# Optimization experiments

Measured on AMD Instinct MI355X. Metric: run time of the kernel, lower is better.

## Reference

```python
import jax, jax.numpy as jnp
import numpy as np
import math

BS, S, D = 2, 2048, 2048
DOWN, UP, H, RD = 512, 1024, 16, 32
HD = D // H            # 128, used only in softmax scale
VD = UP // H           # 64 per-head value dim
CD = UP // H           # 64 per-head content q/k dim
SCALE = math.sqrt(HD) + math.sqrt(RD)


def _rope(x, head_dim):
    # x: [bs, heads, seq, head_dim]; standard rotate-half RoPE
    seq = x.shape[2]
    inv_freq = 1.0 / (10000.0 ** (jnp.arange(0, head_dim, 2, dtype=jnp.float32) / head_dim))
    freqs = jnp.arange(seq, dtype=jnp.float32)[:, None] * inv_freq[None, :]  # [S, hd/2]
    emb = jnp.concatenate([freqs, freqs], axis=-1)                            # [S, hd]
    cos = jnp.cos(emb)[None, None]
    sin = jnp.sin(emb)[None, None]
    x1, x2 = x[..., : head_dim // 2], x[..., head_dim // 2 :]
    rot = jnp.concatenate([-x2, x1], axis=-1)
    return x * cos + rot * sin


def setup_inputs() -> dict:
    key = jax.random.key(0)
    ks = jax.random.split(key, 10)
    sd = 0.02
    inp = {
        'h': jax.random.normal(ks[0], (BS, S, D), jnp.float32),
        'mask': jnp.tril(jnp.ones((1, 1, S, S), jnp.int32)),
        'Wdkv': jax.random.normal(ks[1], (DOWN, D), jnp.float32) * sd,
        'bdkv': jnp.zeros((DOWN,), jnp.float32),
        'Wuk': jax.random.normal(ks[2], (UP, DOWN), jnp.float32) * sd,
        'buk': jnp.zeros((UP,), jnp.float32),
        'Wuv': jax.random.normal(ks[3], (UP, DOWN), jnp.float32) * sd,
        'buv': jnp.zeros((UP,), jnp.float32),
        'Wdq': jax.random.normal(ks[4], (DOWN, D), jnp.float32) * sd,
        'bdq': jnp.zeros((DOWN,), jnp.float32),
        'Wuq': jax.random.normal(ks[5], (UP, DOWN), jnp.float32) * sd,
        'buq': jnp.zeros((UP,), jnp.float32),
        'Wqr': jax.random.normal(ks[6], (RD * H, DOWN), jnp.float32) * sd,
        'bqr': jnp.zeros((RD * H,), jnp.float32),
        'Wkr': jax.random.normal(ks[7], (RD, D), jnp.float32) * sd,
        'bkr': jnp.zeros((RD,), jnp.float32),
        'Wfc': jax.random.normal(ks[8], (D, H * VD), jnp.float32) * sd,
        'bfc': jnp.zeros((D,), jnp.float32),
    }
    return inp


def reference(h, mask, Wdkv, bdkv, Wuk, buk, Wuv, buv, Wdq, bdq, Wuq, buq,
              Wqr, bqr, Wkr, bkr, Wfc, bfc):
    bs, seq, _ = h.shape
    # low-rank KV path
    c_kv = h @ Wdkv.T + bdkv                                   # [bs,S,DOWN]
    k_c = (c_kv @ Wuk.T + buk).reshape(bs, seq, H, CD).transpose(0, 2, 1, 3)
    v_c = (c_kv @ Wuv.T + buv).reshape(bs, seq, H, VD).transpose(0, 2, 1, 3)
    # low-rank Q path
    c_q = h @ Wdq.T + bdq                                      # [bs,S,DOWN]
    q_c = (c_q @ Wuq.T + buq).reshape(bs, seq, H, CD).transpose(0, 2, 1, 3)
    # decoupled RoPE paths
    q_r = _rope((c_q @ Wqr.T + bqr).reshape(bs, seq, H, RD).transpose(0, 2, 1, 3), RD)
    k_r = _rope((h @ Wkr.T + bkr).reshape(bs, seq, 1, RD).transpose(0, 2, 1, 3), RD)
    k_r = jnp.broadcast_to(k_r, (bs, H, seq, RD))              # shared RoPE key across heads
    q = jnp.concatenate([q_c, q_r], axis=-1)                   # [bs,H,S,CD+RD]
    k = jnp.concatenate([k_c, k_r], axis=-1)
    scores = jnp.einsum('bhqd,bhkd->bhqk', q, k)
    # NB: original applies mask BEFORE dividing by scale
    scores = jnp.where(mask == 0, -1e9, scores)
    probs = jax.nn.softmax(scores / SCALE, axis=-1)
    out = jnp.einsum('bhqk,bhkd->bhqd', probs, v_c)            # [bs,H,S,VD]
    out = out.transpose(0, 2, 1, 3).reshape(bs, seq, H * VD)
    return out @ Wfc.T + bfc
```

## Files before the change

### kernel.cpp

```cpp
#include <hip/hip_runtime.h>
#include <hip/hip_bf16.h>
#include <math.h>

typedef unsigned short u16;
typedef __attribute__((ext_vector_type(8))) short bf16x8;
typedef __attribute__((ext_vector_type(4))) float f32x4;
typedef __attribute__((ext_vector_type(16))) float f32x16;

namespace {

constexpr int BS = 2;
constexpr int S = 2048;
constexpr int D = 2048;
constexpr int DOWN = 512;
constexpr int UP = 1024;
constexpr int H = 16;
constexpr int RD = 32;
constexpr int VD = 64;
constexpr int QKD = 96;
constexpr int M = BS * S;
constexpr int N1 = 1152;
constexpr int N2 = 2048;
constexpr int N3 = 1536;

__device__ __forceinline__ float b2f(u16 u) {
  unsigned int x = ((unsigned int)u) << 16;
  return __uint_as_float(x);
}
__device__ __forceinline__ u16 f2b(float f) {
  unsigned int u = __float_as_uint(f);
  u += 0x7fff + ((u >> 16) & 1);
  return (u16)(u >> 16);
}
__device__ __forceinline__ void store_out(float* p, float v) { *p = v; }
__device__ __forceinline__ void store_out(u16* p, float v) { *p = f2b(v); }

__device__ __forceinline__ void async16(const u16* g, u16* lds) {
  __builtin_amdgcn_global_load_lds(
      (const __attribute__((address_space(1))) unsigned int*)g,
      (__attribute__((address_space(3))) unsigned int*)lds, 16, 0, 0);
}

__device__ __forceinline__ float exp2_fast(float x) {
#if __has_builtin(__builtin_amdgcn_exp2f)
  return __builtin_amdgcn_exp2f(x);
#else
  float r;
  asm("v_exp_f32 %0, %1" : "=v"(r) : "v"(x));
  return r;
#endif
}

__device__ __forceinline__ bf16x8 pack8(const float* f) {
  union { __hip_bfloat162 h2[4]; bf16x8 v; } u;
#pragma unroll
  for (int i = 0; i < 4; ++i)
    u.h2[i] = __float22bfloat162_rn(make_float2(f[2 * i], f[2 * i + 1]));
  return u.v;
}

__device__ __forceinline__ f32x4 mfma32(bf16x8 a, bf16x8 b, f32x4 c) {
  return __builtin_amdgcn_mfma_f32_16x16x32_bf16(a, b, c, 0, 0, 0);
}
__device__ __forceinline__ f32x16 mfma3216(bf16x8 a, bf16x8 b, f32x16 c) {
  return __builtin_amdgcn_mfma_f32_32x32x16_bf16(a, b, c, 0, 0, 0);
}

__global__ __launch_bounds__(256) void prep_kernel(
    const float* __restrict__ h, const float* __restrict__ Wdkv,
    const float* __restrict__ Wdq, const float* __restrict__ Wkr,
    const float* __restrict__ Wuk, const float* __restrict__ Wuv,
    const float* __restrict__ Wuq, const float* __restrict__ Wqr,
    const float* __restrict__ Wfc, const float* __restrict__ bdkv,
    const float* __restrict__ bdq, const float* __restrict__ bkr,
    const float* __restrict__ buk, const float* __restrict__ buv,
    const float* __restrict__ buq, const float* __restrict__ bqr,
    u16* __restrict__ hb, u16* __restrict__ Wcat1, u16* __restrict__ Wcat2,
    u16* __restrict__ Wcat3, u16* __restrict__ Wfcb,
    float* __restrict__ bcat1, float* __restrict__ bcat2,
    float* __restrict__ bcat3, float* __restrict__ ct, float* __restrict__ st) {
  const long i = (long)blockIdx.x * 256 + threadIdx.x;
  if (i >= 3630240) return;
  if (i < 3620864) {
    const float* src; u16* dst; long off;
    if      (i < 2097152) { src = h;    dst = hb;              off = i; }
    else if (i < 2359296) { src = Wdkv; dst = Wcat1;           off = i - 2097152; }
    else if (i < 2621440) { src = Wdq;  dst = Wcat1 + 1048576; off = i - 2359296; }
    else if (i < 2637824) { src = Wkr;  dst = Wcat1 + 2097152; off = i - 2621440; }
    else if (i < 2768896) { src = Wuk;  dst = Wcat2;           off = i - 2637824; }
    else if (i < 2899968) { src = Wuv;  dst = Wcat2 + 524288;  off = i - 2768896; }
    else if (i < 3031040) { src = Wuq;  dst = Wcat3;           off = i - 2899968; }
    else if (i < 3096576) { src = Wqr;  dst = Wcat3 + 524288;  off = i - 3031040; }
    else                  { src = Wfc;  dst = Wfcb;            off = i - 3096576; }
    float4 v = ((const float4*)src)[off];
    ushort4 o;
    o.x = f2b(v.x); o.y = f2b(v.y); o.z = f2b(v.z); o.w = f2b(v.w);
    ((ushort4*)dst)[off] = o;
  } else if (i < 3622048) {
    long j0 = (i - 3620864) * 4;
#pragma unroll
    for (int e = 0; e < 4; ++e) {
      long j = j0 + e;
      if (j < N1) {
        float v = 0.f;
        if (j < 512) v = bdkv[j];
        else if (j < 1024) v = bdq[j - 512];
        else if (j < 1056) v = bkr[j - 1024];
        bcat1[j] = v;
      } else if (j < N1 + N2) {
        long jj = j - N1;
        bcat2[jj] = (jj < 1024) ? buk[jj] : buv[jj - 1024];
      } else {
        long jj = j - N1 - N2;
        bcat3[jj] = (jj < 1024) ? buq[jj] : bqr[jj - 1024];
      }
    }
  } else {
    long k0 = (i - 3622048) * 4;
#pragma unroll
    for (int e = 0; e < 4; ++e) {
      long k = k0 + e;
      int s = (int)(k >> 4), r = (int)(k & 15);
      float f = powf(10000.f, -(float)r / 16.f);
      float th = (float)s * f;
      ct[k] = cosf(th);
      st[k] = sinf(th);
    }
  }
}

template <int BN, typename OutT>
__device__ __forceinline__ void gemm_body(
    const u16* __restrict__ A, int lda, const u16* __restrict__ W, int ldw,
    const float* __restrict__ bias, OutT* __restrict__ C, int ldc, int K,
    int m0, int n0) {
  constexpr int NFR = BN / 32;
  __shared__ u16 As[128 * 32];
  __shared__ u16 Bs[BN * 32];
  const int t = threadIdx.x;
  const int lane = t & 63, wave = t >> 6;
  const int wm = (wave >> 1) * 64, wn = (wave & 1) * (BN / 2);
  const int lrow = lane & 15, lk = (lane >> 4) * 8;
  const int srow = lane >> 2, scol = (lane & 3) * 8;
  f32x4 acc[4][NFR] = {};
  for (int k0 = 0; k0 < K; k0 += 32) {
    __syncthreads();
    {
      int r = wave * 32 + srow;
      async16(A + (size_t)(m0 + r) * lda + k0 + scol, As + (wave * 32) * 32);
      async16(A + (size_t)(m0 + r + 16) * lda + k0 + scol,
              As + (wave * 32 + 16) * 32);
    }
    if (BN == 128) {
      int r = wave * 32 + srow;
      async16(W + (size_t)(n0 + r) * ldw + k0 + scol, Bs + (wave * 32) * 32);
      async16(W + (size_t)(n0 + r + 16) * ldw + k0 + scol,
              Bs + (wave * 32 + 16) * 32);
    } else {
      int r = wave * 16 + srow;
      async16(W + (size_t)(n0 + r) * ldw + k0 + scol, Bs + (wave * 16) * 32);
    }
    __syncthreads();
    bf16x8 af[4], bfr[NFR];
#pragma unroll
    for (int i = 0; i < 4; ++i)
      af[i] = *(const bf16x8*)(As + (wm + i * 16 + lrow) * 32 + lk);
#pragma unroll
    for (int i = 0; i < NFR; ++i)
      bfr[i] = *(const bf16x8*)(Bs + (wn + i * 16 + lrow) * 32 + lk);
#pragma unroll
    for (int mi = 0; mi < 4; ++mi)
#pragma unroll
      for (int ni = 0; ni < NFR; ++ni)
        acc[mi][ni] = mfma32(af[mi], bfr[ni], acc[mi][ni]);
  }
#pragma unroll
  for (int mi = 0; mi < 4; ++mi)
#pragma unroll
    for (int ni = 0; ni < NFR; ++ni)
#pragma unroll
      for (int r = 0; r < 4; ++r) {
        int m = m0 + wm + mi * 16 + (lane >> 4) * 4 + r;
        int n = n0 + wn + ni * 16 + lrow;
        store_out(C + (size_t)m * ldc + n, acc[mi][ni][r] + bias[n]);
      }
}

template <int BN, typename OutT>
__global__ __launch_bounds__(256) void gemm_bt_mfma(
    const u16* __restrict__ A, int lda, const u16* __restrict__ W, int ldw,
    const float* __restrict__ bias, OutT* __restrict__ C, int ldc, int K) {
  gemm_body<BN, OutT>(A, lda, W, ldw, bias, C, ldc, K,
                      blockIdx.x * 128, blockIdx.y * BN);
}

__global__ __launch_bounds__(256) void gemm_up_fused(
    const u16* __restrict__ C1v, const u16* __restrict__ Wcat2,
    const u16* __restrict__ Wcat3, const float* __restrict__ bcat2,
    const float* __restrict__ bcat3, u16* __restrict__ C2,
    u16* __restrict__ C3) {
  const int by = blockIdx.y;
  const u16* A;
  const u16* W;
  const float* bias;
  u16* C;
  int ldc, n0;
  if (by < 16) {
    A = C1v; W = Wcat2; bias = bcat2; C = C2; ldc = N2; n0 = by * 128;
  } else {
    A = C1v + DOWN; W = Wcat3; bias = bcat3; C = C3; ldc = N3;
    n0 = (by - 16) * 128;
  }
  gemm_body<128, u16>(A, N1, W, DOWN, bias, C, ldc, DOWN,
                      blockIdx.x * 128, n0);
}

__global__ __launch_bounds__(256) void transpose_kernel(
    const u16* __restrict__ in, int ld_in, u16* __restrict__ outT, int ld_out) {
  __shared__ u16 tile[64][72];
  const int m0 = blockIdx.x * 64, n0 = blockIdx.y * 64;
  const int r = threadIdx.x >> 2, c0 = (threadIdx.x & 3) * 16;
  *(bf16x8*)(&tile[r][c0]) =
      *(const bf16x8*)(in + (size_t)(m0 + r) * ld_in + n0 + c0);
  *(bf16x8*)(&tile[r][c0 + 8]) =
      *(const bf16x8*)(in + (size_t)(m0 + r) * ld_in + n0 + c0 + 8);
  __syncthreads();
  bf16x8 o0, o1;
#pragma unroll
  for (int j = 0; j < 8; ++j) {
    o0[j] = (short)tile[c0 + j][r];
    o1[j] = (short)tile[c0 + 8 + j][r];
  }
  *(bf16x8*)(outT + (size_t)(n0 + r) * ld_out + m0 + c0) = o0;
  *(bf16x8*)(outT + (size_t)(n0 + r) * ld_out + m0 + c0 + 8) = o1;
}

__global__ __launch_bounds__(192) void pack_q_kernel(
    const u16* __restrict__ qc, const u16* __restrict__ qr,
    const float* __restrict__ ct, const float* __restrict__ st,
    u16* __restrict__ Qp) {
  const int t = threadIdx.x;
  const int sub = (t >= 96) ? 1 : 0;
  const int d = t - sub * 96;
  const int s = blockIdx.x * 2 + sub, h = blockIdx.y, b = blockIdx.z;
  const float sc = 1.44269504088896f / (sqrtf(128.f) + sqrtf(32.f));
  float val;
  if (d < 64) {
    val = b2f(qc[(size_t)(b * S + s) * N3 + h * VD + d]);
  } else {
    int r = d - 64;
    const u16* qrow = qr + (size_t)(b * S + s) * N3 + h * RD;
    float x = b2f(qrow[r]), xp = b2f(qrow[r ^ 16]);
    float c = ct[s * 16 + (r & 15)], sn = st[s * 16 + (r & 15)];
    val = (r < 16) ? (x * c - xp * sn) : (x * c + xp * sn);
  }
  Qp[((size_t)(b * H + h) * S + s) * QKD + d] = f2b(val * sc);
}

__global__ __launch_bounds__(192) void pack_k_kernel(
    const u16* __restrict__ kc,
    const u16* __restrict__ kr,
    const float* __restrict__ ct, const float* __restrict__ st,
    u16* __restrict__ Kp) {
  const int t = threadIdx.x;
  const int sub = (t >= 96) ? 1 : 0;
  const int d = t - sub * 96;
  const int s = blockIdx.x * 2 + sub, h = blockIdx.y, b = blockIdx.z;
  float val;
  if (d < 64) {
    val = b2f(kc[(size_t)(b * S + s) * N2 + h * VD + d]);
  } else {
    int r = d - 64;
    const u16* krow = kr + (size_t)(b * S + s) * N1;
    float x = b2f(krow[r]), xp = b2f(krow[r ^ 16]);
    float c = ct[s * 16 + (r & 15)], sn = st[s * 16 + (r & 15)];
    val = (r < 16) ? (x * c - xp * sn) : (x * c + xp * sn);
  }
  Kp[((size_t)(b * H + h) * S + s) * QKD + d] = f2b(val);
}

__global__ __launch_bounds__(256) void attn_mfma(
    const u16* __restrict__ Qp, const u16* __restrict__ Kp,
    const u16* __restrict__ Vt, u16* __restrict__ attnb) {
  const int t = threadIdx.x, wave = t >> 6, lane = t & 63;
  const int l31 = lane & 31, hw = lane >> 5;
  const int bh = blockIdx.x & 31;
  const int b = bh >> 4, h = bh & 15;
  const int j = blockIdx.x >> 5;
  const int qgroup = (j < 8) ? (15 - j) : (j - 8);
  const int q0w = qgroup * 128 + wave * 32;
  const size_t hbo = (size_t)bh * S;

  bf16x8 qf[6];
  {
    const u16* qrow = Qp + (hbo + q0w + l31) * QKD + hw * 8;
#pragma unroll
    for (int c = 0; c < 6; ++c) qf[c] = *(const bf16x8*)(qrow + c * 16);
  }
  f32x16 O0 = {0,0,0,0,0,0,0,0,0,0,0,0,0,0,0,0};
  f32x16 O1 = {0,0,0,0,0,0,0,0,0,0,0,0,0,0,0,0};
  float lsum = 0.f;
  const int q_abs = q0w + l31;
  const u16* vb0 = Vt + ((size_t)(h * VD + l31)) * M + (size_t)b * S + 8 * hw;

  for (int k0 = 0; k0 < q0w + 32; k0 += 32) {
    const u16* kb = Kp + (hbo + k0 + l31) * QKD + hw * 8;
    f32x16 s = {0,0,0,0,0,0,0,0,0,0,0,0,0,0,0,0};
#pragma unroll
    for (int c = 0; c < 6; ++c) {
      bf16x8 kf = *(const bf16x8*)(kb + c * 16);
      s = mfma3216(kf, qf[c], s);
    }
    float e[16];
    if (k0 + 31 > q0w) {
#pragma unroll
      for (int r = 0; r < 16; ++r) {
        int key_abs = k0 + (r & 3) + 8 * (r >> 2) + 4 * hw;
        float v = exp2_fast(s[r]);
        e[r] = (key_abs <= q_abs) ? v : 0.f;
      }
    } else {
#pragma unroll
      for (int r = 0; r < 16; ++r) e[r] = exp2_fast(s[r]);
    }
#pragma unroll
    for (int r = 0; r < 16; ++r) lsum += e[r];
    float x[16];
#pragma unroll
    for (int r = 0; r < 16; ++r) x[r] = __shfl_xor(e[r], 32);
    float f0[8], f1[8];
#pragma unroll
    for (int jj = 0; jj < 4; ++jj) {
      f0[jj]     = hw ? x[jj + 4]  : e[jj];
      f0[jj + 4] = hw ? e[jj + 4]  : x[jj];
      f1[jj]     = hw ? x[jj + 12] : e[jj + 8];
      f1[jj + 4] = hw ? e[jj + 12] : x[jj + 8];
    }
    bf16x8 pa0 = pack8(f0);
    bf16x8 pa1 = pack8(f1);
    bf16x8 vf00 = *(const bf16x8*)(vb0 + k0);
    bf16x8 vf01 = *(const bf16x8*)(vb0 + k0 + 16);
    bf16x8 vf10 = *(const bf16x8*)(vb0 + (size_t)32 * M + k0);
    bf16x8 vf11 = *(const bf16x8*)(vb0 + (size_t)32 * M + k0 + 16);
    O0 = mfma3216(pa0, vf00, O0);
    O0 = mfma3216(pa1, vf01, O0);
    O1 = mfma3216(pa0, vf10, O1);
    O1 = mfma3216(pa1, vf11, O1);
  }

  float tot = lsum + __shfl_xor(lsum, 32);
  u16* ob = attnb + (size_t)b * S * UP + h * VD;
#pragma unroll
  for (int r = 0; r < 16; ++r) {
    int rowq = (r & 3) + 8 * (r >> 2) + 4 * hw;
    float linv = 1.f / __shfl(tot, rowq);
    size_t rowoff = (size_t)(q0w + rowq) * UP;
    ob[rowoff + l31] = f2b(O0[r] * linv);
    ob[rowoff + 32 + l31] = f2b(O1[r] * linv);
  }
}

}

extern "C" void kernel_launch(void* const* d_in, const int* in_sizes, int n_in,
                              void* d_out, int out_size, void* d_ws, size_t ws_size,
                              hipStream_t stream) {
  const float* h    = (const float*)d_in[0];
  const float* Wdkv = (const float*)d_in[2];
  const float* bdkv = (const float*)d_in[3];
  const float* Wuk  = (const float*)d_in[4];
  const float* buk  = (const float*)d_in[5];
  const float* Wuv  = (const float*)d_in[6];
  const float* buv  = (const float*)d_in[7];
  const float* Wdq  = (const float*)d_in[8];
  const float* bdq  = (const float*)d_in[9];
  const float* Wuq  = (const float*)d_in[10];
  const float* buq  = (const float*)d_in[11];
  const float* Wqr  = (const float*)d_in[12];
  const float* bqr  = (const float*)d_in[13];
  const float* Wkr  = (const float*)d_in[14];
  const float* bkr  = (const float*)d_in[15];
  const float* Wfc  = (const float*)d_in[16];
  const float* bfc  = (const float*)d_in[17];
  float* out = (float*)d_out;

  u16* p = (u16*)d_ws;
  u16* hb    = p; p += (size_t)M * D;
  u16* Wcat1 = p; p += (size_t)N1 * D;
  u16* Wcat2 = p; p += (size_t)N2 * DOWN;
  u16* Wcat3 = p; p += (size_t)N3 * DOWN;
  u16* Wfcb  = p; p += (size_t)D * UP;
  u16* C1    = p; p += (size_t)M * N1;
  u16* C2    = p; p += (size_t)M * N2;
  u16* C3    = p; p += (size_t)M * N3;
  u16* Qp    = p; p += 6291456;
  u16* Kp    = p; p += 6291456;
  u16* Vt    = p; p += (size_t)UP * M;
  float* bcat1 = (float*)p; p += 2 * N1;
  float* bcat2 = (float*)p; p += 2 * N2;
  float* bcat3 = (float*)p; p += 2 * N3;
  float* ct = (float*)p; p += 2 * S * 16;
  float* st = (float*)p; p += 2 * S * 16;
  u16* attnb = C1;

  prep_kernel<<<dim3(14181), 256, 0, stream>>>(
      h, Wdkv, Wdq, Wkr, Wuk, Wuv, Wuq, Wqr, Wfc,
      bdkv, bdq, bkr, buk, buv, buq, bqr,
      hb, Wcat1, Wcat2, Wcat3, Wfcb, bcat1, bcat2, bcat3, ct, st);

  gemm_bt_mfma<64, u16><<<dim3(M / 128, N1 / 64), 256, 0, stream>>>(
      hb, D, Wcat1, D, bcat1, C1, N1, D);
  gemm_up_fused<<<dim3(M / 128, 28), 256, 0, stream>>>(
      C1, Wcat2, Wcat3, bcat2, bcat3, C2, C3);

  pack_q_kernel<<<dim3(S / 2, H, BS), 192, 0, stream>>>(
      C3, C3 + UP, ct, st, Qp);
  pack_k_kernel<<<dim3(S / 2, H, BS), 192, 0, stream>>>(
      C2, C1 + 2 * DOWN, ct, st, Kp);
  transpose_kernel<<<dim3(M / 64, UP / 64), 256, 0, stream>>>(
      C2 + UP, N2, Vt, M);

  attn_mfma<<<dim3(512), 256, 0, stream>>>(Qp, Kp, Vt, attnb);

  gemm_bt_mfma<64, float><<<dim3(M / 128, D / 64), 256, 0, stream>>>(
      attnb, UP, Wfcb, UP, bfc, out, D, UP);
}
```

Measured before the change: 363.4 us.

## Split attention keys across waves with LDS reduction and permlane swap

Each block now handles a single 32-query tile, and its four waves take interleaved 32-key chunks. The partial outputs and row sums are combined through shared memory at the end, and the launch grows from 512 to 2048 blocks to raise parallelism and balance the causal workload. The cross-half shuffle used to repack probabilities for the PV MFMA is replaced by bf16 packing plus v_permlane32_swap. K fragments are prefetched one iteration ahead. The cost is an LDS reduction and a block-wide barrier, and each block now reloads the same Q tile, so Q is read redundantly.

```diff
diff --git a/kernel.cpp b/kernel.cpp
--- a/kernel.cpp
+++ b/kernel.cpp
@@ -51,12 +51,13 @@
 #endif
 }
 
-__device__ __forceinline__ bf16x8 pack8(const float* f) {
-  union { __hip_bfloat162 h2[4]; bf16x8 v; } u;
-#pragma unroll
-  for (int i = 0; i < 4; ++i)
-    u.h2[i] = __float22bfloat162_rn(make_float2(f[2 * i], f[2 * i + 1]));
-  return u.v;
+__device__ __forceinline__ unsigned pkbf(float a, float b) {
+  union { __hip_bfloat162 h; unsigned u; } c;
+  c.h = __float22bfloat162_rn(make_float2(a, b));
+  return c.u;
+}
+__device__ __forceinline__ void plswap(unsigned& a, unsigned& b) {
+  asm("v_permlane32_swap_b32 %0, %1" : "+v"(a), "+v"(b));
 }
 
 __device__ __forceinline__ f32x4 mfma32(bf16x8 a, bf16x8 b, f32x4 c) {
@@ -279,17 +280,18 @@
   Kp[((size_t)(b * H + h) * S + s) * QKD + d] = f2b(val);
 }
 
-__global__ __launch_bounds__(256) void attn_mfma(
+__global__ __launch_bounds__(256, 4) void attn_mfma(
     const u16* __restrict__ Qp, const u16* __restrict__ Kp,
     const u16* __restrict__ Vt, u16* __restrict__ attnb) {
   const int t = threadIdx.x, wave = t >> 6, lane = t & 63;
   const int l31 = lane & 31, hw = lane >> 5;
   const int bh = blockIdx.x & 31;
   const int b = bh >> 4, h = bh & 15;
-  const int j = blockIdx.x >> 5;
-  const int qgroup = (j < 8) ? (15 - j) : (j - 8);
-  const int q0w = qgroup * 128 + wave * 32;
+  const int tile = 63 - (blockIdx.x >> 5);
+  const int q0w = tile * 32;
   const size_t hbo = (size_t)bh * S;
+
+  __shared__ float red[3][64][33];
 
   bf16x8 qf[6];
   {
@@ -303,60 +305,83 @@
   const int q_abs = q0w + l31;
   const u16* vb0 = Vt + ((size_t)(h * VD + l31)) * M + (size_t)b * S + 8 * hw;
 
-  for (int k0 = 0; k0 < q0w + 32; k0 += 32) {
-    const u16* kb = Kp + (hbo + k0 + l31) * QKD + hw * 8;
+  bf16x8 kf[6];
+  {
+    const u16* kb = Kp + (hbo + wave * 32 + l31) * QKD + hw * 8;
+#pragma unroll
+    for (int c = 0; c < 6; ++c) kf[c] = *(const bf16x8*)(kb + c * 16);
+  }
+
+  for (int m = wave; m <= tile; m += 4) {
+    const int k0 = m * 32;
     f32x16 s = {0,0,0,0,0,0,0,0,0,0,0,0,0,0,0,0};
 #pragma unroll
-    for (int c = 0; c < 6; ++c) {
-      bf16x8 kf = *(const bf16x8*)(kb + c * 16);
-      s = mfma3216(kf, qf[c], s);
-    }
-    float e[16];
-    if (k0 + 31 > q0w) {
-#pragma unroll
-      for (int r = 0; r < 16; ++r) {
-        int key_abs = k0 + (r & 3) + 8 * (r >> 2) + 4 * hw;
-        float v = exp2_fast(s[r]);
-        e[r] = (key_abs <= q_abs) ? v : 0.f;
-      }
-    } else {
-#pragma unroll
-      for (int r = 0; r < 16; ++r) e[r] = exp2_fast(s[r]);
-    }
-#pragma unroll
-    for (int r = 0; r < 16; ++r) lsum += e[r];
-    float x[16];
-#pragma unroll
-    for (int r = 0; r < 16; ++r) x[r] = __shfl_xor(e[r], 32);
-    float f0[8], f1[8];
-#pragma unroll
-    for (int jj = 0; jj < 4; ++jj) {
-      f0[jj]     = hw ? x[jj + 4]  : e[jj];
-      f0[jj + 4] = hw ? e[jj + 4]  : x[jj];
-      f1[jj]     = hw ? x[jj + 12] : e[jj + 8];
-      f1[jj + 4] = hw ? e[jj + 12] : x[jj + 8];
-    }
-    bf16x8 pa0 = pack8(f0);
-    bf16x8 pa1 = pack8(f1);
+    for (int c = 0; c < 6; ++c) s = mfma3216(kf[c], qf[c], s);
+    if (m + 4 <= tile) {
+      const u16* kb = Kp + (hbo + (size_t)(m + 4) * 32 + l31) * QKD + hw * 8;
+#pragma unroll
+      for (int c = 0; c < 6; ++c) kf[c] = *(const bf16x8*)(kb + c * 16);
+    }
     bf16x8 vf00 = *(const bf16x8*)(vb0 + k0);
     bf16x8 vf01 = *(const bf16x8*)(vb0 + k0 + 16);
     bf16x8 vf10 = *(const bf16x8*)(vb0 + (size_t)32 * M + k0);
     bf16x8 vf11 = *(const bf16x8*)(vb0 + (size_t)32 * M + k0 + 16);
-    O0 = mfma3216(pa0, vf00, O0);
-    O0 = mfma3216(pa1, vf01, O0);
-    O1 = mfma3216(pa0, vf10, O1);
-    O1 = mfma3216(pa1, vf11, O1);
-  }
-
-  float tot = lsum + __shfl_xor(lsum, 32);
-  u16* ob = attnb + (size_t)b * S * UP + h * VD;
-#pragma unroll
-  for (int r = 0; r < 16; ++r) {
-    int rowq = (r & 3) + 8 * (r >> 2) + 4 * hw;
-    float linv = 1.f / __shfl(tot, rowq);
-    size_t rowoff = (size_t)(q0w + rowq) * UP;
-    ob[rowoff + l31] = f2b(O0[r] * linv);
-    ob[rowoff + 32 + l31] = f2b(O1[r] * linv);
+    if (m == tile) {
+#pragma unroll
+      for (int r = 0; r < 16; ++r) {
+        int key_abs = k0 + (r & 3) + 8 * (r >> 2) + 4 * hw;
+        float v = exp2_fast(s[r]);
+        s[r] = (key_abs <= q_abs) ? v : 0.f;
+      }
+    } else {
+#pragma unroll
+      for (int r = 0; r < 16; ++r) s[r] = exp2_fast(s[r]);
+    }
+#pragma unroll
+    for (int r = 0; r < 16; ++r) lsum += s[r];
+    unsigned w0 = pkbf(s[0], s[1]),   w1 = pkbf(s[2], s[3]);
+    unsigned w2 = pkbf(s[4], s[5]),   w3 = pkbf(s[6], s[7]);
+    unsigned w4 = pkbf(s[8], s[9]),   w5 = pkbf(s[10], s[11]);
+    unsigned w6 = pkbf(s[12], s[13]), w7 = pkbf(s[14], s[15]);
+    plswap(w0, w2); plswap(w1, w3); plswap(w4, w6); plswap(w5, w7);
+    union { unsigned u[4]; bf16x8 v; } ua, ub;
+    ua.u[0] = w0; ua.u[1] = w1; ua.u[2] = w2; ua.u[3] = w3;
+    ub.u[0] = w4; ub.u[1] = w5; ub.u[2] = w6; ub.u[3] = w7;
+    O0 = mfma3216(ua.v, vf00, O0);
+    O0 = mfma3216(ub.v, vf01, O0);
+    O1 = mfma3216(ua.v, vf10, O1);
+    O1 = mfma3216(ub.v, vf11, O1);
+  }
+
+  if (wave > 0) {
+#pragma unroll
+    for (int r = 0; r < 16; ++r) {
+      red[wave - 1][lane][r] = O0[r];
+      red[wave - 1][lane][16 + r] = O1[r];
+    }
+    red[wave - 1][lane][32] = lsum;
+  }
+  __syncthreads();
+  if (wave == 0) {
+#pragma unroll
+    for (int w = 0; w < 3; ++w) {
+#pragma unroll
+      for (int r = 0; r < 16; ++r) {
+        O0[r] += red[w][lane][r];
+        O1[r] += red[w][lane][16 + r];
+      }
+      lsum += red[w][lane][32];
+    }
+    float tot = lsum + __shfl_xor(lsum, 32);
+    u16* ob = attnb + (size_t)b * S * UP + h * VD;
+#pragma unroll
+    for (int r = 0; r < 16; ++r) {
+      int rowq = (r & 3) + 8 * (r >> 2) + 4 * hw;
+      float linv = 1.f / __shfl(tot, rowq);
+      size_t rowoff = (size_t)(q0w + rowq) * UP;
+      ob[rowoff + l31] = f2b(O0[r] * linv);
+      ob[rowoff + 32 + l31] = f2b(O1[r] * linv);
+    }
   }
 }
 
@@ -420,7 +445,7 @@
   transpose_kernel<<<dim3(M / 64, UP / 64), 256, 0, stream>>>(
       C2 + UP, N2, Vt, M);
 
-  attn_mfma<<<dim3(512), 256, 0, stream>>>(Qp, Kp, Vt, attnb);
+  attn_mfma<<<dim3(2048), 256, 0, stream>>>(Qp, Kp, Vt, attnb);
 
   gemm_bt_mfma<64, float><<<dim3(M / 128, D / 64), 256, 0, stream>>>(
       attnb, UP, Wfcb, UP, bfc, out, D, UP);
```

New measurement: 346.8 us. -4.6%, faster.
